# Kernel tuning notes

Hardware: AMD Instinct MI355X
Metric: run time of the kernel (lower is better)

Reference implementation:

```python
import jax, jax.numpy as jnp
import numpy as np

N = 16384
IN_F = 256
OUT_F = 128
EDGE_PROB = 0.002  # ~33 neighbors per node on average


def setup_inputs() -> dict:
    key = jax.random.key(0)
    k_a, k_h, k_w = jax.random.split(key, 3)
    # Sparse-ish dense adjacency: nonzero entries where uniform < EDGE_PROB,
    # matching the original code's `A[i, j] != 0` branching.
    u = jax.random.uniform(k_a, (N, N), dtype=jnp.float32)
    A = jnp.where(u < EDGE_PROB, u + 0.5, 0.0).astype(jnp.float32)
    H = jax.random.normal(k_h, (N, IN_F), dtype=jnp.float32)
    # kaiming_uniform_(a=sqrt(5)) on (out, in): bound = 1/sqrt(in)
    bound = 1.0 / np.sqrt(IN_F)
    kernel = jax.random.uniform(k_w, (OUT_F, IN_F), dtype=jnp.float32,
                                minval=-bound, maxval=bound)
    return {"A": A, "H": H, "kernel": kernel}


def reference(A, H, kernel):
    # Faithful vectorization of the nested-loop forward:
    #   aggregate_i = (sum_{j : A[i,j] != 0} H[j]) / (deg_i + 1)
    #   H_out[i]   = aggregate_i @ kernel.T
    mask = (A != 0).astype(H.dtype)                 # [N, N]
    deg_plus_one = jnp.sum(mask, axis=1) + 1.0       # n_neighbors starts at 1
    agg = (mask @ H) / deg_plus_one[:, None]         # [N, in_f]
    return agg @ kernel.T                            # [N, out_f]
```

## Files before the change

### kernel.cpp

```cpp
#include <hip/hip_runtime.h>

#define NNODE 16384
#define IN_F  256
#define OUT_F 128
#define ROWS  8
#define MAXNB 256

__global__ __launch_bounds__(256, 8) void gcn_fused_kernel(
    const float* __restrict__ A,
    const float* __restrict__ H,
    const float* __restrict__ W,
    float* __restrict__ out)
{
    __shared__ int   s_cnt[ROWS];
    __shared__ int   s_idx[ROWS][MAXNB];
    __shared__ float s_agg[ROWS][IN_F];
    __shared__ float s_part[OUT_F][ROWS];

    const int t = threadIdx.x;
    const int row0 = blockIdx.x * ROWS;

    if (t < ROWS) s_cnt[t] = 0;
    __syncthreads();

    for (int r = 0; r < ROWS; ++r) {
        const float4* A4 = reinterpret_cast<const float4*>(
            A + (size_t)(row0 + r) * NNODE);
        #pragma unroll
        for (int k = 0; k < NNODE / (256 * 4); ++k) {
            float4 v = A4[k * 256 + t];
            int j = (k * 256 + t) * 4;
            if (v.x != 0.f) { int p = atomicAdd(&s_cnt[r], 1); if (p < MAXNB) s_idx[r][p] = j;     }
            if (v.y != 0.f) { int p = atomicAdd(&s_cnt[r], 1); if (p < MAXNB) s_idx[r][p] = j + 1; }
            if (v.z != 0.f) { int p = atomicAdd(&s_cnt[r], 1); if (p < MAXNB) s_idx[r][p] = j + 2; }
            if (v.w != 0.f) { int p = atomicAdd(&s_cnt[r], 1); if (p < MAXNB) s_idx[r][p] = j + 3; }
        }
    }
    __syncthreads();

    for (int r = 0; r < ROWS; ++r) {
        const int cnt = s_cnt[r];
        float acc = 0.f;
        for (int k = 0; k < cnt; ++k) {
            const int j = s_idx[r][k];
            acc += H[(size_t)j * IN_F + t];
        }
        s_agg[r][t] = acc / (float)(cnt + 1);
    }
    __syncthreads();

    const int o    = t & (OUT_F - 1);
    const int half = t >> 7;
    float acc[ROWS];
    #pragma unroll
    for (int r = 0; r < ROWS; ++r) acc[r] = 0.f;

    const float* Wrow = W + (size_t)o * IN_F + half * (IN_F / 2);
    for (int k = 0; k < IN_F / 2; ++k) {
        const float wv = Wrow[k];
        const int c = half * (IN_F / 2) + k;
        #pragma unroll
        for (int r = 0; r < ROWS; ++r) acc[r] += wv * s_agg[r][c];
    }

    if (half == 1) {
        #pragma unroll
        for (int r = 0; r < ROWS; ++r) s_part[o][r] = acc[r];
    }
    __syncthreads();
    if (half == 0) {
        #pragma unroll
        for (int r = 0; r < ROWS; ++r)
            out[(size_t)(row0 + r) * OUT_F + o] = acc[r] + s_part[o][r];
    }
}

extern "C" void kernel_launch(void* const* d_in, const int* in_sizes, int n_in,
                              void* d_out, int out_size, void* d_ws, size_t ws_size,
                              hipStream_t stream) {
    const float* A = (const float*)d_in[0];
    const float* H = (const float*)d_in[1];
    const float* W = (const float*)d_in[2];
    float* out = (float*)d_out;

    dim3 grid(NNODE / ROWS);
    dim3 block(256);
    gcn_fused_kernel<<<grid, block, 0, stream>>>(A, H, W, out);
}
```

Before: 1.411 ms.

## Assign one wave per row for scan and gather, vectorize H and W loads

Cuts rows per block from 8 to 4 and gives each 64-lane wave its own adjacency row to scan, so the rows are processed concurrently rather than one after another by the whole block. The block-wide barrier between scan and gather goes away because each wave gathers its own row's neighbors. Gather reads H as float4 with four independent accumulators to increase memory-level parallelism. The W loads become float4, and the s_part array is padded to avoid LDS bank conflicts. In exchange the grid doubles, so W is reloaded by twice as many blocks, and the ordering of the float sums changes.

```diff
diff --git a/kernel.cpp b/kernel.cpp
--- a/kernel.cpp
+++ b/kernel.cpp
@@ -3,10 +3,10 @@
 #define NNODE 16384
 #define IN_F  256
 #define OUT_F 128
-#define ROWS  8
+#define ROWS  4
 #define MAXNB 256
 
-__global__ __launch_bounds__(256, 8) void gcn_fused_kernel(
+__global__ __launch_bounds__(256, 4) void gcn_fused_kernel(
     const float* __restrict__ A,
     const float* __restrict__ H,
     const float* __restrict__ W,
@@ -15,52 +15,83 @@
     __shared__ int   s_cnt[ROWS];
     __shared__ int   s_idx[ROWS][MAXNB];
     __shared__ float s_agg[ROWS][IN_F];
-    __shared__ float s_part[OUT_F][ROWS];
+    __shared__ float s_part[OUT_F][ROWS + 1];
 
-    const int t = threadIdx.x;
+    const int t    = threadIdx.x;
+    const int wave = t >> 6;
+    const int lane = t & 63;
     const int row0 = blockIdx.x * ROWS;
 
     if (t < ROWS) s_cnt[t] = 0;
     __syncthreads();
 
-    for (int r = 0; r < ROWS; ++r) {
-        const float4* A4 = reinterpret_cast<const float4*>(
-            A + (size_t)(row0 + r) * NNODE);
-        #pragma unroll
-        for (int k = 0; k < NNODE / (256 * 4); ++k) {
-            float4 v = A4[k * 256 + t];
-            int j = (k * 256 + t) * 4;
-            if (v.x != 0.f) { int p = atomicAdd(&s_cnt[r], 1); if (p < MAXNB) s_idx[r][p] = j;     }
-            if (v.y != 0.f) { int p = atomicAdd(&s_cnt[r], 1); if (p < MAXNB) s_idx[r][p] = j + 1; }
-            if (v.z != 0.f) { int p = atomicAdd(&s_cnt[r], 1); if (p < MAXNB) s_idx[r][p] = j + 2; }
-            if (v.w != 0.f) { int p = atomicAdd(&s_cnt[r], 1); if (p < MAXNB) s_idx[r][p] = j + 3; }
-        }
+    const float4* A4 = reinterpret_cast<const float4*>(
+        A + (size_t)(row0 + wave) * NNODE);
+
+#define PROC(v, kk)                                                              \
+    {                                                                            \
+        int j = ((kk) * 64 + lane) * 4;                                          \
+        if ((v).x != 0.f) { int p = atomicAdd(&s_cnt[wave], 1); if (p < MAXNB) s_idx[wave][p] = j;     } \
+        if ((v).y != 0.f) { int p = atomicAdd(&s_cnt[wave], 1); if (p < MAXNB) s_idx[wave][p] = j + 1; } \
+        if ((v).z != 0.f) { int p = atomicAdd(&s_cnt[wave], 1); if (p < MAXNB) s_idx[wave][p] = j + 2; } \
+        if ((v).w != 0.f) { int p = atomicAdd(&s_cnt[wave], 1); if (p < MAXNB) s_idx[wave][p] = j + 3; } \
     }
-    __syncthreads();
 
-    for (int r = 0; r < ROWS; ++r) {
-        const int cnt = s_cnt[r];
-        float acc = 0.f;
-        for (int k = 0; k < cnt; ++k) {
-            const int j = s_idx[r][k];
-            acc += H[(size_t)j * IN_F + t];
-        }
-        s_agg[r][t] = acc / (float)(cnt + 1);
+    for (int k = 0; k < NNODE / 4 / 64; k += 4) {
+        float4 v0 = A4[(k + 0) * 64 + lane];
+        float4 v1 = A4[(k + 1) * 64 + lane];
+        float4 v2 = A4[(k + 2) * 64 + lane];
+        float4 v3 = A4[(k + 3) * 64 + lane];
+        PROC(v0, k + 0) PROC(v1, k + 1) PROC(v2, k + 2) PROC(v3, k + 3)
     }
+#undef PROC
+
+    const float4* H4 = reinterpret_cast<const float4*>(H);
+    int cnt = s_cnt[wave];
+    if (cnt > MAXNB) cnt = MAXNB;
+
+    float4 a0 = {0,0,0,0}, a1 = a0, a2 = a0, a3 = a0;
+    int k = 0;
+    for (; k + 4 <= cnt; k += 4) {
+        int j0 = s_idx[wave][k + 0], j1 = s_idx[wave][k + 1];
+        int j2 = s_idx[wave][k + 2], j3 = s_idx[wave][k + 3];
+        float4 v0 = H4[(size_t)j0 * 64 + lane];
+        float4 v1 = H4[(size_t)j1 * 64 + lane];
+        float4 v2 = H4[(size_t)j2 * 64 + lane];
+        float4 v3 = H4[(size_t)j3 * 64 + lane];
+        a0.x += v0.x; a0.y += v0.y; a0.z += v0.z; a0.w += v0.w;
+        a1.x += v1.x; a1.y += v1.y; a1.z += v1.z; a1.w += v1.w;
+        a2.x += v2.x; a2.y += v2.y; a2.z += v2.z; a2.w += v2.w;
+        a3.x += v3.x; a3.y += v3.y; a3.z += v3.z; a3.w += v3.w;
+    }
+    for (; k < cnt; ++k) {
+        int j = s_idx[wave][k];
+        float4 v = H4[(size_t)j * 64 + lane];
+        a0.x += v.x; a0.y += v.y; a0.z += v.z; a0.w += v.w;
+    }
+    const float inv = 1.f / (float)(cnt + 1);
+    float4 agg;
+    agg.x = (a0.x + a1.x + a2.x + a3.x) * inv;
+    agg.y = (a0.y + a1.y + a2.y + a3.y) * inv;
+    agg.z = (a0.z + a1.z + a2.z + a3.z) * inv;
+    agg.w = (a0.w + a1.w + a2.w + a3.w) * inv;
+    *reinterpret_cast<float4*>(&s_agg[wave][lane * 4]) = agg;
     __syncthreads();
 
     const int o    = t & (OUT_F - 1);
     const int half = t >> 7;
-    float acc[ROWS];
-    #pragma unroll
-    for (int r = 0; r < ROWS; ++r) acc[r] = 0.f;
+    float acc[ROWS] = {0.f, 0.f, 0.f, 0.f};
 
-    const float* Wrow = W + (size_t)o * IN_F + half * (IN_F / 2);
-    for (int k = 0; k < IN_F / 2; ++k) {
-        const float wv = Wrow[k];
-        const int c = half * (IN_F / 2) + k;
+    const float4* W4 = reinterpret_cast<const float4*>(
+        W + (size_t)o * IN_F + half * (IN_F / 2));
+    for (int kk = 0; kk < IN_F / 2 / 4; ++kk) {
+        float4 wv = W4[kk];
+        const int c = half * (IN_F / 2) + kk * 4;
         #pragma unroll
-        for (int r = 0; r < ROWS; ++r) acc[r] += wv * s_agg[r][c];
+        for (int r = 0; r < ROWS; ++r) {
+            float4 g = *reinterpret_cast<const float4*>(&s_agg[r][c]);
+            acc[r] += wv.x * g.x + wv.y * g.y + wv.z * g.z + wv.w * g.w;
+        }
     }
 
     if (half == 1) {
```

Result: no change. 1.416 ms (+0.3%).

## Split GCN into per-row scan/aggregate kernel and separate register-tiled GEMM

Applied to the files above, without the earlier changes.

Splits the fused kernel into two. The first handles one row per block: it streams the dense adjacency row with batched nontemporal vector loads to collect neighbour indices, then gathers H rows with float4 loads split across four waves. The aggregate is written to workspace, and a second kernel runs a 4x4 register-tiled GEMM against W. The intent is more memory-level parallelism on the 1 GiB adjacency scan and a cheaper projection, at the cost of an extra global round trip for the aggregate and a second launch.

```diff
diff --git a/kernel.cpp b/kernel.cpp
--- a/kernel.cpp
+++ b/kernel.cpp
@@ -3,76 +3,127 @@
 #define NNODE 16384
 #define IN_F  256
 #define OUT_F 128
-#define ROWS  8
 #define MAXNB 256
 
-__global__ __launch_bounds__(256, 8) void gcn_fused_kernel(
+typedef float vfloat4 __attribute__((ext_vector_type(4)));
+
+__global__ __launch_bounds__(256, 4) void gcn_scan_aggregate(
     const float* __restrict__ A,
     const float* __restrict__ H,
+    float* __restrict__ agg)
+{
+    __shared__ int   s_cnt;
+    __shared__ int   s_idx[MAXNB];
+    __shared__ float s_part[4][IN_F];
+
+    const int t    = threadIdx.x;
+    const int wave = t >> 6;
+    const int lane = t & 63;
+    const int row  = blockIdx.x;
+
+    if (t == 0) s_cnt = 0;
+    __syncthreads();
+
+    const vfloat4* A4 = reinterpret_cast<const vfloat4*>(
+        A + (size_t)row * NNODE);
+
+#define PROC(v, idx)                                                             \
+    {                                                                            \
+        int j = (idx) * 4;                                                       \
+        if ((v).x != 0.f) { int p = atomicAdd(&s_cnt, 1); if (p < MAXNB) s_idx[p] = j;     } \
+        if ((v).y != 0.f) { int p = atomicAdd(&s_cnt, 1); if (p < MAXNB) s_idx[p] = j + 1; } \
+        if ((v).z != 0.f) { int p = atomicAdd(&s_cnt, 1); if (p < MAXNB) s_idx[p] = j + 2; } \
+        if ((v).w != 0.f) { int p = atomicAdd(&s_cnt, 1); if (p < MAXNB) s_idx[p] = j + 3; } \
+    }
+
+    #pragma unroll
+    for (int kk = 0; kk < 16; kk += 8) {
+        vfloat4 v0 = __builtin_nontemporal_load(&A4[(kk + 0) * 256 + t]);
+        vfloat4 v1 = __builtin_nontemporal_load(&A4[(kk + 1) * 256 + t]);
+        vfloat4 v2 = __builtin_nontemporal_load(&A4[(kk + 2) * 256 + t]);
+        vfloat4 v3 = __builtin_nontemporal_load(&A4[(kk + 3) * 256 + t]);
+        vfloat4 v4 = __builtin_nontemporal_load(&A4[(kk + 4) * 256 + t]);
+        vfloat4 v5 = __builtin_nontemporal_load(&A4[(kk + 5) * 256 + t]);
+        vfloat4 v6 = __builtin_nontemporal_load(&A4[(kk + 6) * 256 + t]);
+        vfloat4 v7 = __builtin_nontemporal_load(&A4[(kk + 7) * 256 + t]);
+        PROC(v0, (kk + 0) * 256 + t) PROC(v1, (kk + 1) * 256 + t)
+        PROC(v2, (kk + 2) * 256 + t) PROC(v3, (kk + 3) * 256 + t)
+        PROC(v4, (kk + 4) * 256 + t) PROC(v5, (kk + 5) * 256 + t)
+        PROC(v6, (kk + 6) * 256 + t) PROC(v7, (kk + 7) * 256 + t)
+    }
+#undef PROC
+    __syncthreads();
+
+    const int cnt  = s_cnt;
+    const int cntc = cnt < MAXNB ? cnt : MAXNB;
+
+    const float4* H4 = reinterpret_cast<const float4*>(H);
+    float4 acc = {0.f, 0.f, 0.f, 0.f};
+    int k = wave;
+    for (; k + 4 < cntc; k += 8) {
+        int j0 = s_idx[k];
+        int j1 = s_idx[k + 4];
+        float4 v0 = H4[(size_t)j0 * 64 + lane];
+        float4 v1 = H4[(size_t)j1 * 64 + lane];
+        acc.x += v0.x + v1.x; acc.y += v0.y + v1.y;
+        acc.z += v0.z + v1.z; acc.w += v0.w + v1.w;
+    }
+    if (k < cntc) {
+        float4 v = H4[(size_t)s_idx[k] * 64 + lane];
+        acc.x += v.x; acc.y += v.y; acc.z += v.z; acc.w += v.w;
+    }
+    *reinterpret_cast<float4*>(&s_part[wave][lane * 4]) = acc;
+    __syncthreads();
+
+    const float inv = 1.f / (float)(cnt + 1);
+    float sum = s_part[0][t] + s_part[1][t] + s_part[2][t] + s_part[3][t];
+    agg[(size_t)row * IN_F + t] = sum * inv;
+}
+
+__global__ __launch_bounds__(256, 4) void gcn_gemm(
+    const float* __restrict__ agg,
     const float* __restrict__ W,
     float* __restrict__ out)
 {
-    __shared__ int   s_cnt[ROWS];
-    __shared__ int   s_idx[ROWS][MAXNB];
-    __shared__ float s_agg[ROWS][IN_F];
-    __shared__ float s_part[OUT_F][ROWS];
+    const int t  = threadIdx.x;
+    const int og = t & 31;
+    const int rg = t >> 5;
+    const int r0 = blockIdx.x * 32 + rg * 4;
 
-    const int t = threadIdx.x;
-    const int row0 = blockIdx.x * ROWS;
+    const float4* A4 = reinterpret_cast<const float4*>(agg);
+    const float4* W4 = reinterpret_cast<const float4*>(W);
 
-    if (t < ROWS) s_cnt[t] = 0;
-    __syncthreads();
+    float acc[4][4];
+    #pragma unroll
+    for (int i = 0; i < 4; ++i)
+        #pragma unroll
+        for (int j = 0; j < 4; ++j) acc[i][j] = 0.f;
 
-    for (int r = 0; r < ROWS; ++r) {
-        const float4* A4 = reinterpret_cast<const float4*>(
-            A + (size_t)(row0 + r) * NNODE);
+    #pragma unroll 2
+    for (int q = 0; q < IN_F / 4; ++q) {
+        float4 a0 = A4[(size_t)(r0 + 0) * 64 + q];
+        float4 a1 = A4[(size_t)(r0 + 1) * 64 + q];
+        float4 a2 = A4[(size_t)(r0 + 2) * 64 + q];
+        float4 a3 = A4[(size_t)(r0 + 3) * 64 + q];
+        float4 w0 = W4[(size_t)(og +  0) * 64 + q];
+        float4 w1 = W4[(size_t)(og + 32) * 64 + q];
+        float4 w2 = W4[(size_t)(og + 64) * 64 + q];
+        float4 w3 = W4[(size_t)(og + 96) * 64 + q];
+        float4 ar[4] = {a0, a1, a2, a3};
+        float4 wr[4] = {w0, w1, w2, w3};
         #pragma unroll
-        for (int k = 0; k < NNODE / (256 * 4); ++k) {
-            float4 v = A4[k * 256 + t];
-            int j = (k * 256 + t) * 4;
-            if (v.x != 0.f) { int p = atomicAdd(&s_cnt[r], 1); if (p < MAXNB) s_idx[r][p] = j;     }
-            if (v.y != 0.f) { int p = atomicAdd(&s_cnt[r], 1); if (p < MAXNB) s_idx[r][p] = j + 1; }
-            if (v.z != 0.f) { int p = atomicAdd(&s_cnt[r], 1); if (p < MAXNB) s_idx[r][p] = j + 2; }
-            if (v.w != 0.f) { int p = atomicAdd(&s_cnt[r], 1); if (p < MAXNB) s_idx[r][p] = j + 3; }
-        }
-    }
-    __syncthreads();
-
-    for (int r = 0; r < ROWS; ++r) {
-        const int cnt = s_cnt[r];
-        float acc = 0.f;
-        for (int k = 0; k < cnt; ++k) {
-            const int j = s_idx[r][k];
-            acc += H[(size_t)j * IN_F + t];
-        }
-        s_agg[r][t] = acc / (float)(cnt + 1);
-    }
-    __syncthreads();
-
-    const int o    = t & (OUT_F - 1);
-    const int half = t >> 7;
-    float acc[ROWS];
-    #pragma unroll
-    for (int r = 0; r < ROWS; ++r) acc[r] = 0.f;
-
-    const float* Wrow = W + (size_t)o * IN_F + half * (IN_F / 2);
-    for (int k = 0; k < IN_F / 2; ++k) {
-        const float wv = Wrow[k];
-        const int c = half * (IN_F / 2) + k;
-        #pragma unroll
-        for (int r = 0; r < ROWS; ++r) acc[r] += wv * s_agg[r][c];
+        for (int i = 0; i < 4; ++i)
+            #pragma unroll
+            for (int j = 0; j < 4; ++j)
+                acc[i][j] += ar[i].x * wr[j].x + ar[i].y * wr[j].y +
+                             ar[i].z * wr[j].z + ar[i].w * wr[j].w;
     }
 
-    if (half == 1) {
+    #pragma unroll
+    for (int i = 0; i < 4; ++i)
         #pragma unroll
-        for (int r = 0; r < ROWS; ++r) s_part[o][r] = acc[r];
-    }
-    __syncthreads();
-    if (half == 0) {
-        #pragma unroll
-        for (int r = 0; r < ROWS; ++r)
-            out[(size_t)(row0 + r) * OUT_F + o] = acc[r] + s_part[o][r];
-    }
+        for (int j = 0; j < 4; ++j)
+            out[(size_t)(r0 + i) * OUT_F + og + j * 32] = acc[i][j];
 }
 
 extern "C" void kernel_launch(void* const* d_in, const int* in_sizes, int n_in,
@@ -82,8 +133,8 @@
     const float* H = (const float*)d_in[1];
     const float* W = (const float*)d_in[2];
     float* out = (float*)d_out;
+    float* agg = (float*)d_ws;
 
-    dim3 grid(NNODE / ROWS);
-    dim3 block(256);
-    gcn_fused_kernel<<<grid, block, 0, stream>>>(A, H, W, out);
+    gcn_scan_aggregate<<<dim3(NNODE), dim3(256), 0, stream>>>(A, H, agg);
+    gcn_gemm<<<dim3(NNODE / 32), dim3(256), 0, stream>>>(agg, W, out);
 }
```

Result: slower. 1.440 ms (+2.0%).
